# Performance work log

Measured on AMD Instinct MI355X. Metric: run time of the kernel, lower is better.

Reference implementation:

```python
import jax, jax.numpy as jnp
import numpy as np

RNN = 512
ENC = 512
HID = 512
ATT_SIZE = 196
B = 1024


def setup_inputs() -> dict:
    key = jax.random.key(0)
    ks = jax.random.split(key, 20)
    s = 0.02
    d = {
        "h": jax.random.normal(ks[0], (B, RNN), jnp.float32),
        "sentinel": jax.random.normal(ks[1], (B, RNN), jnp.float32),
        "att_feats": jax.random.normal(ks[2], (B, ATT_SIZE, RNN), jnp.float32),
        "W_ctx2att": jax.random.normal(ks[3], (RNN, HID), jnp.float32) * s,
        "b_ctx2att": jnp.zeros((HID,), jnp.float32),
        "W_sl": jax.random.normal(ks[4], (RNN, ENC), jnp.float32) * s,
        "b_sl": jnp.zeros((ENC,), jnp.float32),
        "W_se": jax.random.normal(ks[5], (ENC, HID), jnp.float32) * s,
        "b_se": jnp.zeros((HID,), jnp.float32),
        "W_hl": jax.random.normal(ks[6], (RNN, ENC), jnp.float32) * s,
        "b_hl": jnp.zeros((ENC,), jnp.float32),
        "W_he": jax.random.normal(ks[7], (ENC, HID), jnp.float32) * s,
        "b_he": jnp.zeros((HID,), jnp.float32),
        "W_alpha": jax.random.normal(ks[8], (HID, 1), jnp.float32) * s,
        "b_alpha": jnp.zeros((1,), jnp.float32),
        "W_att2h": jax.random.normal(ks[9], (RNN, RNN), jnp.float32) * s,
        "b_att2h": jnp.zeros((RNN,), jnp.float32),
    }
    return d


def reference(h, sentinel, att_feats, W_ctx2att, b_ctx2att, W_sl, b_sl,
              W_se, b_se, W_hl, b_hl, W_he, b_he, W_alpha, b_alpha,
              W_att2h, b_att2h):
    # Eval mode: dropout is identity.
    # Project attention features: [B, 196, HID]
    p_att = jnp.einsum("bsd,dh->bsh", att_feats, W_ctx2att) + b_ctx2att
    # Sentinel branch
    sent_lin = jax.nn.relu(sentinel @ W_sl + b_sl)          # [B, ENC]
    sent_emb = sent_lin @ W_se + b_se                       # [B, HID]
    # Hidden-state branch
    h_lin = jnp.tanh(h @ W_hl + b_hl)                       # [B, ENC]
    h_emb = h_lin @ W_he + b_he                             # [B, HID]
    # Concat sentinel with visual features: [B, 197, *]
    img_all = jnp.concatenate([sent_lin[:, None, :], att_feats], axis=1)
    img_all_embed = jnp.concatenate([sent_emb[:, None, :], p_att], axis=1)
    # Additive attention scores over 197 positions
    hA = jnp.tanh(img_all_embed + h_emb[:, None, :])        # [B, 197, HID]
    scores = (jnp.einsum("bsh,ho->bso", hA, W_alpha) + b_alpha)[..., 0]  # [B, 197]
    alpha = jax.nn.softmax(scores, axis=-1)
    # Weighted context
    cHat = jnp.einsum("bs,bsd->bd", alpha, img_all)          # [B, RNN]
    atten_out = cHat + h_lin
    out = jnp.tanh(atten_out @ W_att2h + b_att2h)            # [B, RNN]
    return out
```

## Files before the change

### kernel.cpp

```cpp
#include <hip/hip_runtime.h>
#include <hip/hip_bf16.h>

#define KDIM 512
#define NDIM 512
#define ATT  196
#define NB   1024

typedef __attribute__((ext_vector_type(8))) short bf16x8;
typedef __attribute__((ext_vector_type(8))) unsigned short ushort8;
typedef __attribute__((ext_vector_type(4))) float f32x4;

typedef const __attribute__((address_space(1))) unsigned int gas_uint;
typedef __attribute__((address_space(3))) unsigned int las_uint;

__device__ __forceinline__ void gload16(const void* g, void* l) {
    __builtin_amdgcn_global_load_lds((gas_uint*)g, (las_uint*)l, 16, 0, 0);
}

__device__ __forceinline__ float fast_tanh(float x) {
    x = fminf(15.f, fmaxf(-15.f, x));
    float t = __expf(2.f * x);
    return (t - 1.f) / (t + 1.f);
}

__device__ __forceinline__ unsigned short f2bf(float x) {
    union { float f; unsigned u; } v; v.f = x;
    unsigned r = v.u + 0x7FFF + ((v.u >> 16) & 1);
    return (unsigned short)(r >> 16);
}

__device__ __forceinline__ unsigned pk2(float a, float b) {
    __hip_bfloat162 h = __float22bfloat162_rn(float2{a, b});
    union { __hip_bfloat162 h2; unsigned u; } c; c.h2 = h;
    return c.u;
}

__global__ __launch_bounds__(256) void prep_weights(
        const float* __restrict__ W0, const float* __restrict__ W1,
        const float* __restrict__ W2, const float* __restrict__ W3,
        const float* __restrict__ W4, const float* __restrict__ W5,
        unsigned short* __restrict__ Wt) {
    int w = blockIdx.x >> 6;
    int t = blockIdx.x & 63;
    int k0 = (t >> 3) << 6, n0 = (t & 7) << 6;
    const float* W = (w == 0) ? W0 : (w == 1) ? W1 : (w == 2) ? W2 :
                     (w == 3) ? W3 : (w == 4) ? W4 : W5;
    __shared__ float tile[64][65];
    int tid = threadIdx.x;
    int nc = tid & 15, kr = tid >> 4;
#pragma unroll
    for (int i = 0; i < 4; ++i) {
        int k = kr + i * 16;
        float4 v = *(const float4*)&W[(size_t)(k0 + k) * NDIM + n0 + nc * 4];
        tile[k][nc * 4 + 0] = v.x; tile[k][nc * 4 + 1] = v.y;
        tile[k][nc * 4 + 2] = v.z; tile[k][nc * 4 + 3] = v.w;
    }
    __syncthreads();
    int n = tid >> 2, ks = tid & 3;
    ushort8 v0, v1;
#pragma unroll
    for (int j = 0; j < 8; ++j) v0[j] = f2bf(tile[ks * 16 + j][n]);
#pragma unroll
    for (int j = 0; j < 8; ++j) v1[j] = f2bf(tile[ks * 16 + 8 + j][n]);
    size_t base = ((size_t)w << 18) + (size_t)(n0 + n) * KDIM + k0 + ks * 16;
    *(ushort8*)&Wt[base] = v0;
    *(ushort8*)&Wt[base + 8] = v1;
}

__global__ __launch_bounds__(256) void gemm64(
        const float* __restrict__ A0, const unsigned short* __restrict__ W0,
        const float* __restrict__ bia0, float* __restrict__ O0, int act0,
        const float* __restrict__ A1, const unsigned short* __restrict__ W1,
        const float* __restrict__ bia1, float* __restrict__ O1, int act1) {
    const int op = blockIdx.y;
    const float* A = op ? A1 : A0;
    const unsigned short* Bt = op ? W1 : W0;
    const float* bias = op ? bia1 : bia0;
    float* out = op ? O1 : O0;
    const int act = op ? act1 : act0;

    __shared__ unsigned short A_lds[2][64 * 32];
    __shared__ unsigned short B_lds[2][128 * 32];

    const int tid = threadIdx.x;
    const int gm0 = (blockIdx.x >> 2) * 64, gn0 = (blockIdx.x & 3) * 128;
    const int wid = tid >> 6, lane = tid & 63;
    const int wm = wid >> 1, wn = wid & 1;
    const int lr = lane & 15, lk = lane >> 4;

    const int arow = tid >> 2, akc = tid & 3;
    const float* aptr = A + (size_t)(gm0 + arow) * KDIM + akc * 8;
    const int aoff = arow * 32 + ((akc ^ ((arow >> 1) & 3)) << 3);

    auto stageB = [&](int kt, int buf) {
#pragma unroll
        for (int j = 0; j < 2; ++j) {
            int c = tid + j * 256;
            int col = c >> 2, slot = c & 3;
            const unsigned short* src = Bt + (size_t)(gn0 + col) * KDIM +
                                        ((slot ^ ((col >> 1) & 3)) << 3) + kt * 32;
            gload16(src, &B_lds[buf][c * 8]);
        }
    };

    f32x4 acc[2][4] = {};

    {
        float4 x0 = *(const float4*)aptr;
        float4 x1 = *(const float4*)(aptr + 4);
        stageB(0, 0);
        uint4 p;
        p.x = pk2(x0.x, x0.y); p.y = pk2(x0.z, x0.w);
        p.z = pk2(x1.x, x1.y); p.w = pk2(x1.z, x1.w);
        *(uint4*)&A_lds[0][aoff] = p;
    }
    __syncthreads();

    const int swk = ((lk ^ ((lr >> 1) & 3)) << 3);
    for (int kt = 0; kt < 16; ++kt) {
        const int buf = kt & 1;
        float4 x0, x1;
        if (kt < 15) {
            const float* ap = aptr + (kt + 1) * 32;
            x0 = *(const float4*)ap;
            x1 = *(const float4*)(ap + 4);
            stageB(kt + 1, buf ^ 1);
        }
        bf16x8 af[2], bfr[4];
#pragma unroll
        for (int m = 0; m < 2; ++m)
            af[m] = *(const bf16x8*)&A_lds[buf][(wm * 32 + m * 16 + lr) * 32 + swk];
#pragma unroll
        for (int n = 0; n < 4; ++n)
            bfr[n] = *(const bf16x8*)&B_lds[buf][(wn * 64 + n * 16 + lr) * 32 + swk];
#pragma unroll
        for (int m = 0; m < 2; ++m)
#pragma unroll
            for (int n = 0; n < 4; ++n)
                acc[m][n] = __builtin_amdgcn_mfma_f32_16x16x32_bf16(af[m], bfr[n], acc[m][n], 0, 0, 0);
        if (kt < 15) {
            uint4 p;
            p.x = pk2(x0.x, x0.y); p.y = pk2(x0.z, x0.w);
            p.z = pk2(x1.x, x1.y); p.w = pk2(x1.z, x1.w);
            *(uint4*)&A_lds[buf ^ 1][aoff] = p;
        }
        __syncthreads();
    }

#pragma unroll
    for (int m = 0; m < 2; ++m)
#pragma unroll
        for (int n = 0; n < 4; ++n) {
            int col = gn0 + wn * 64 + n * 16 + lr;
            float bsv = bias[col];
#pragma unroll
            for (int r = 0; r < 4; ++r) {
                int row = gm0 + wm * 32 + m * 16 + lk * 4 + r;
                float v = acc[m][n][r] + bsv;
                if (act == 0) v = fmaxf(v, 0.f);
                else if (act == 1) v = fast_tanh(v);
                out[(size_t)row * NDIM + col] = v;
            }
        }
}

__launch_bounds__(256, 3)
__global__ void gemm_score(const float* __restrict__ A,
                           const unsigned short* __restrict__ Bt,
                           const float* __restrict__ b_ctx,
                           const float* __restrict__ h_emb,
                           const float* __restrict__ Walpha,
                           float* __restrict__ score) {
    __shared__ unsigned short A_lds[3][128 * 32];
    __shared__ unsigned short B_lds[3][128 * 32];
    __shared__ float ch_s[2][128];
    __shared__ float wa_s[128];
    __shared__ float s_red[2][128];

    const int tid  = threadIdx.x;
    const int bidx = blockIdx.x;
    const int xcd  = bidx & 7, u = bidx >> 3;
    const int mblk = xcd * 196 + (u >> 2), nblk = u & 3;
    const int gm0  = mblk * 128, gn0 = nblk * 128;

    const int wid = tid >> 6, lane = tid & 63;
    const int wm  = wid >> 1, wn = wid & 1;
    const int lr  = lane & 15, lk = lane >> 4;

    const int arow = tid >> 1, ahalf = tid & 1;
    const float* aptr = A + (size_t)(gm0 + arow) * KDIM + ahalf * 16;
    const int skc0  = (ahalf * 2) ^ ((arow >> 1) & 3);
    const int aoff0 = arow * 32 + skc0 * 8;
    const int aoff1 = arow * 32 + (skc0 ^ 1) * 8;

    const int c1 = tid + 256;
    const int bcol0 = tid >> 2, bk0 = (tid & 3) ^ ((bcol0 >> 1) & 3);
    const int bcol1 = c1 >> 2,  bk1 = (c1 & 3) ^ ((bcol1 >> 1) & 3);
    const unsigned short* bsrc0 = Bt + (size_t)(gn0 + bcol0) * KDIM + bk0 * 8;
    const unsigned short* bsrc1 = Bt + (size_t)(gn0 + bcol1) * KDIM + bk1 * 8;

    auto issueB = [&](int kt, int buf) {
        gload16(bsrc0 + kt * 32, &B_lds[buf][tid * 8]);
        gload16(bsrc1 + kt * 32, &B_lds[buf][c1 * 8]);
    };
    auto loadA = [&](int kt, float4* x) {
        const float* ap = aptr + kt * 32;
        x[0] = *(const float4*)(ap);
        x[1] = *(const float4*)(ap + 4);
        x[2] = *(const float4*)(ap + 8);
        x[3] = *(const float4*)(ap + 12);
    };
    auto writeA = [&](float4* x, int buf) {
        uint4 p0, p1;
        p0.x = pk2(x[0].x, x[0].y); p0.y = pk2(x[0].z, x[0].w);
        p0.z = pk2(x[1].x, x[1].y); p0.w = pk2(x[1].z, x[1].w);
        p1.x = pk2(x[2].x, x[2].y); p1.y = pk2(x[2].z, x[2].w);
        p1.z = pk2(x[3].x, x[3].y); p1.w = pk2(x[3].z, x[3].w);
        *(uint4*)&A_lds[buf][aoff0] = p0;
        *(uint4*)&A_lds[buf][aoff1] = p1;
    };

    f32x4 acc[4][4] = {};
    float4 xa[4], xb[4];
    const int swk = ((lk ^ ((lr >> 1) & 3)) << 3);

    loadA(0, xa);
    issueB(0, 0);
    writeA(xa, 0);
    loadA(1, xa);
    issueB(1, 1);
    asm volatile("s_waitcnt vmcnt(6) lgkmcnt(0)" ::: "memory");
    __builtin_amdgcn_sched_barrier(0);
    __builtin_amdgcn_s_barrier();
    __builtin_amdgcn_sched_barrier(0);

    auto body = [&](int t, int bT, int bT1, int bT2, float4* xc, float4* xn) {
        if (t + 2 < 16) {
            loadA(t + 2, xn);
            issueB(t + 2, bT2);
        }
        __builtin_amdgcn_sched_barrier(0);
        bf16x8 af[4], bfr[4];
#pragma unroll
        for (int m = 0; m < 4; ++m)
            af[m] = *(const bf16x8*)&A_lds[bT][(wm * 64 + m * 16 + lr) * 32 + swk];
#pragma unroll
        for (int n = 0; n < 4; ++n)
            bfr[n] = *(const bf16x8*)&B_lds[bT][(wn * 64 + n * 16 + lr) * 32 + swk];
#pragma unroll
        for (int m = 0; m < 4; ++m)
#pragma unroll
            for (int n = 0; n < 4; ++n)
                acc[m][n] = __builtin_amdgcn_mfma_f32_16x16x32_bf16(af[m], bfr[n], acc[m][n], 0, 0, 0);
        if (t + 1 < 16) writeA(xc, bT1);
        if (t < 15) {
            if (t + 2 < 16) {
                asm volatile("s_waitcnt vmcnt(6) lgkmcnt(0)" ::: "memory");
            } else {
                asm volatile("s_waitcnt vmcnt(0) lgkmcnt(0)" ::: "memory");
            }
            __builtin_amdgcn_sched_barrier(0);
            __builtin_amdgcn_s_barrier();
            __builtin_amdgcn_sched_barrier(0);
        }
    };

    int q0 = 0;
#pragma unroll 1
    for (int tt = 0; tt < 16; tt += 2) {
        int q1 = (q0 == 2) ? 0 : q0 + 1;
        int q2 = (q1 == 2) ? 0 : q1 + 1;
        int q3 = (q2 == 2) ? 0 : q2 + 1;
        body(tt,     q0, q1, q2, xa, xb);
        body(tt + 1, q1, q2, q3, xb, xa);
        q0 = q2;
    }

    const int bb0 = gm0 / ATT;
    {
        int j = tid >> 7, cloc = tid & 127;
        int bb = bb0 + j; if (bb > NB - 1) bb = NB - 1;
        ch_s[j][cloc] = b_ctx[gn0 + cloc] + h_emb[(size_t)bb * NDIM + gn0 + cloc];
        if (tid < 128) wa_s[tid] = Walpha[gn0 + tid];
    }
    __syncthreads();

    const int bsplit = (bb0 + 1) * ATT;
#pragma unroll
    for (int m = 0; m < 4; ++m) {
#pragma unroll
        for (int r = 0; r < 4; ++r) {
            int rloc = wm * 64 + m * 16 + lk * 4 + r;
            int rg = gm0 + rloc;
            int sel = (rg >= bsplit) ? 1 : 0;
            float sum = 0.f;
#pragma unroll
            for (int n = 0; n < 4; ++n) {
                int cloc = wn * 64 + n * 16 + lr;
                sum += fast_tanh(acc[m][n][r] + ch_s[sel][cloc]) * wa_s[cloc];
            }
            sum += __shfl_xor(sum, 1);
            sum += __shfl_xor(sum, 2);
            sum += __shfl_xor(sum, 4);
            sum += __shfl_xor(sum, 8);
            if (lr == 0) s_red[wn][rloc] = sum;
        }
    }
    __syncthreads();
    if (tid < 128) {
        float tot = s_red[0][tid] + s_red[1][tid];
        int rg = gm0 + tid;
        int sel = (rg >= bsplit) ? 1 : 0;
        int bb = bb0 + sel;
        atomicAdd(&score[(size_t)bb * 197 + (rg - bb * ATT) + 1], tot);
    }
}

__global__ __launch_bounds__(256) void softmax_chat(
        const float* __restrict__ score, const float* __restrict__ sent_emb,
        const float* __restrict__ h_emb, const float* __restrict__ Walpha,
        const float* __restrict__ sent_lin, const float* __restrict__ h_lin,
        const float* __restrict__ att, float* __restrict__ atten_out) {
    int b = blockIdx.x, tid = threadIdx.x;
    __shared__ float al[200];
    __shared__ float r4[4];

    float2 se = ((const float2*)(sent_emb + (size_t)b * NDIM))[tid];
    float2 he = ((const float2*)(h_emb + (size_t)b * NDIM))[tid];
    float2 wa = ((const float2*)Walpha)[tid];
    float val = fast_tanh(se.x + he.x) * wa.x + fast_tanh(se.y + he.y) * wa.y;
#pragma unroll
    for (int o = 32; o; o >>= 1) val += __shfl_xor(val, o);
    if ((tid & 63) == 0) r4[tid >> 6] = val;
    __syncthreads();
    float ssent = r4[0] + r4[1] + r4[2] + r4[3];
    __syncthreads();

    float v = -1e30f;
    if (tid < 197) v = (tid == 0) ? ssent : score[(size_t)b * 197 + tid];
    float m = v;
#pragma unroll
    for (int o = 32; o; o >>= 1) m = fmaxf(m, __shfl_xor(m, o));
    if ((tid & 63) == 0) r4[tid >> 6] = m;
    __syncthreads();
    m = fmaxf(fmaxf(r4[0], r4[1]), fmaxf(r4[2], r4[3]));
    __syncthreads();
    float e = (tid < 197) ? __expf(v - m) : 0.f;
    float s = e;
#pragma unroll
    for (int o = 32; o; o >>= 1) s += __shfl_xor(s, o);
    if ((tid & 63) == 0) r4[tid >> 6] = s;
    __syncthreads();
    s = r4[0] + r4[1] + r4[2] + r4[3];
    if (tid < 197) al[tid] = e / s;
    __syncthreads();

    const float2* af = (const float2*)(att + (size_t)b * ATT * KDIM);
    float2 a0 = ((const float2*)(sent_lin + (size_t)b * KDIM))[tid];
    float w0 = al[0];
    float2 accv; accv.x = w0 * a0.x; accv.y = w0 * a0.y;
#pragma unroll 14
    for (int ss = 0; ss < ATT; ++ss) {
        float w = al[ss + 1];
        float2 x = af[(size_t)ss * 256 + tid];
        accv.x += w * x.x; accv.y += w * x.y;
    }
    float2 hl = ((const float2*)(h_lin + (size_t)b * KDIM))[tid];
    accv.x += hl.x; accv.y += hl.y;
    ((float2*)(atten_out + (size_t)b * KDIM))[tid] = accv;
}

extern "C" void kernel_launch(void* const* d_in, const int* in_sizes, int n_in,
                              void* d_out, int out_size, void* d_ws, size_t ws_size,
                              hipStream_t stream) {
    const float* h     = (const float*)d_in[0];
    const float* sent  = (const float*)d_in[1];
    const float* att   = (const float*)d_in[2];
    const float* W_ctx = (const float*)d_in[3];
    const float* b_ctx = (const float*)d_in[4];
    const float* W_sl  = (const float*)d_in[5];
    const float* b_sl  = (const float*)d_in[6];
    const float* W_se  = (const float*)d_in[7];
    const float* b_se  = (const float*)d_in[8];
    const float* W_hl  = (const float*)d_in[9];
    const float* b_hl  = (const float*)d_in[10];
    const float* W_he  = (const float*)d_in[11];
    const float* b_he  = (const float*)d_in[12];
    const float* W_al  = (const float*)d_in[13];
    const float* W_a2h = (const float*)d_in[15];
    const float* b_a2h = (const float*)d_in[16];
    float* out = (float*)d_out;

    char* ws = (char*)d_ws;
    unsigned short* Wt = (unsigned short*)ws;
    float* sent_lin = (float*)(ws + 6u * 512 * 1024);
    float* h_lin    = sent_lin + (size_t)NB * 512;
    float* h_emb    = h_lin    + (size_t)NB * 512;
    float* sent_emb = h_emb    + (size_t)NB * 512;
    float* scorebuf = sent_emb + (size_t)NB * 512;
    float* atten    = scorebuf + (size_t)NB * 197;

    const size_t WSZ = 512 * 512;
    prep_weights<<<384, 256, 0, stream>>>(W_sl, W_hl, W_he, W_ctx, W_a2h, W_se, Wt);
    hipMemsetAsync(scorebuf, 0, (size_t)NB * 197 * sizeof(float), stream);

    gemm64<<<dim3(64, 2), 256, 0, stream>>>(
        sent, Wt + 0 * WSZ, b_sl, sent_lin, 0,
        h,    Wt + 1 * WSZ, b_hl, h_lin,    1);
    gemm64<<<dim3(64, 2), 256, 0, stream>>>(
        h_lin,    Wt + 2 * WSZ, b_he, h_emb,    2,
        sent_lin, Wt + 5 * WSZ, b_se, sent_emb, 2);

    gemm_score<<<6272, 256, 0, stream>>>(att, Wt + 3 * WSZ, b_ctx, h_emb, W_al, scorebuf);

    softmax_chat<<<NB, 256, 0, stream>>>(scorebuf, sent_emb, h_emb, W_al,
                                         sent_lin, h_lin, att, atten);

    gemm64<<<dim3(64, 1), 256, 0, stream>>>(
        atten, Wt + 4 * WSZ, b_a2h, out, 1,
        atten, Wt + 4 * WSZ, b_a2h, out, 1);
}
```

Measured before the change: 391.5 us.

## Keep full W_ctx2att column tile resident in LDS, loop blocks over four M-tiles

The score GEMM now loads the entire 512x128 bf16 weight slice for its N block into LDS once (128 KB) and reuses it across four consecutive 128-row M tiles. Each block runs a persistent-style loop with double-buffered A staging and an epilogue every 16 k-steps, and the grid shrinks by four times. This removes the repeated weight reloads and per-block prologue costs. In exchange occupancy drops to one block per CU and the weight load is exposed at block start without overlap.

```diff
diff --git a/kernel.cpp b/kernel.cpp
--- a/kernel.cpp
+++ b/kernel.cpp
@@ -164,155 +164,161 @@
         }
 }
 
-__launch_bounds__(256, 3)
+__launch_bounds__(256, 1)
 __global__ void gemm_score(const float* __restrict__ A,
                            const unsigned short* __restrict__ Bt,
                            const float* __restrict__ b_ctx,
                            const float* __restrict__ h_emb,
                            const float* __restrict__ Walpha,
                            float* __restrict__ score) {
-    __shared__ unsigned short A_lds[3][128 * 32];
-    __shared__ unsigned short B_lds[3][128 * 32];
-    __shared__ float ch_s[2][128];
-    __shared__ float wa_s[128];
+    __shared__ unsigned short B_res[16 * 4096];
+    __shared__ unsigned short A_buf[2][128 * 32];
     __shared__ float s_red[2][128];
 
-    const int tid  = threadIdx.x;
-    const int bidx = blockIdx.x;
-    const int xcd  = bidx & 7, u = bidx >> 3;
-    const int mblk = xcd * 196 + (u >> 2), nblk = u & 3;
-    const int gm0  = mblk * 128, gn0 = nblk * 128;
+    const int tid = threadIdx.x;
+    const int bid = blockIdx.x;
+    const int xcd = bid & 7, v = bid >> 3;
+    const int nblk = v & 3, gl = v >> 2;
+    const int group = xcd * 49 + gl;
+    const int gbase = group * 512;
+    const int gn0 = nblk * 128;
 
     const int wid = tid >> 6, lane = tid & 63;
-    const int wm  = wid >> 1, wn = wid & 1;
-    const int lr  = lane & 15, lk = lane >> 4;
+    const int wm = wid >> 1, wn = wid & 1;
+    const int lr = lane & 15, lk = lane >> 4;
+    const int swk = ((lk ^ ((lr >> 1) & 3)) << 3);
 
     const int arow = tid >> 1, ahalf = tid & 1;
-    const float* aptr = A + (size_t)(gm0 + arow) * KDIM + ahalf * 16;
-    const int skc0  = (ahalf * 2) ^ ((arow >> 1) & 3);
+    const int skc0 = (ahalf * 2) ^ ((arow >> 1) & 3);
     const int aoff0 = arow * 32 + skc0 * 8;
     const int aoff1 = arow * 32 + (skc0 ^ 1) * 8;
 
-    const int c1 = tid + 256;
-    const int bcol0 = tid >> 2, bk0 = (tid & 3) ^ ((bcol0 >> 1) & 3);
-    const int bcol1 = c1 >> 2,  bk1 = (c1 & 3) ^ ((bcol1 >> 1) & 3);
-    const unsigned short* bsrc0 = Bt + (size_t)(gn0 + bcol0) * KDIM + bk0 * 8;
-    const unsigned short* bsrc1 = Bt + (size_t)(gn0 + bcol1) * KDIM + bk1 * 8;
-
-    auto issueB = [&](int kt, int buf) {
-        gload16(bsrc0 + kt * 32, &B_lds[buf][tid * 8]);
-        gload16(bsrc1 + kt * 32, &B_lds[buf][c1 * 8]);
-    };
-    auto loadA = [&](int kt, float4* x) {
-        const float* ap = aptr + kt * 32;
-        x[0] = *(const float4*)(ap);
-        x[1] = *(const float4*)(ap + 4);
-        x[2] = *(const float4*)(ap + 8);
-        x[3] = *(const float4*)(ap + 12);
-    };
-    auto writeA = [&](float4* x, int buf) {
+    int cols[4];
+    float wav[4], bcv[4];
+#pragma unroll
+    for (int n = 0; n < 4; ++n) {
+        cols[n] = gn0 + wn * 64 + n * 16 + lr;
+        wav[n] = Walpha[cols[n]];
+        bcv[n] = b_ctx[cols[n]];
+    }
+    asm volatile("s_waitcnt vmcnt(0)" ::: "memory");
+    __builtin_amdgcn_sched_barrier(0);
+
+#pragma unroll
+    for (int i = 0; i < 32; ++i) {
+        int c = tid + i * 256;
+        int kt = c >> 9, w = c & 511;
+        int col = w >> 2, slot = w & 3;
+        int kc = slot ^ ((col >> 1) & 3);
+        gload16(Bt + (size_t)(gn0 + col) * KDIM + kt * 32 + kc * 8, &B_res[c * 8]);
+    }
+    __builtin_amdgcn_sched_barrier(0);
+
+    f32x4 acc[4][4] = {};
+    float4 xe0, xe1, xe2, xe3, xo0, xo1, xo2, xo3;
+
+    auto LOADA = [&](int s, float4& y0, float4& y1, float4& y2, float4& y3) {
+        const float* ap = A + (size_t)(gbase + ((s >> 4) << 7) + arow) * KDIM +
+                          ((s & 15) << 5) + ahalf * 16;
+        y0 = *(const float4*)(ap);
+        y1 = *(const float4*)(ap + 4);
+        y2 = *(const float4*)(ap + 8);
+        y3 = *(const float4*)(ap + 12);
+    };
+    auto CVTW = [&](const float4& y0, const float4& y1, const float4& y2,
+                    const float4& y3, int buf) {
         uint4 p0, p1;
-        p0.x = pk2(x[0].x, x[0].y); p0.y = pk2(x[0].z, x[0].w);
-        p0.z = pk2(x[1].x, x[1].y); p0.w = pk2(x[1].z, x[1].w);
-        p1.x = pk2(x[2].x, x[2].y); p1.y = pk2(x[2].z, x[2].w);
-        p1.z = pk2(x[3].x, x[3].y); p1.w = pk2(x[3].z, x[3].w);
-        *(uint4*)&A_lds[buf][aoff0] = p0;
-        *(uint4*)&A_lds[buf][aoff1] = p1;
-    };
-
-    f32x4 acc[4][4] = {};
-    float4 xa[4], xb[4];
-    const int swk = ((lk ^ ((lr >> 1) & 3)) << 3);
-
-    loadA(0, xa);
-    issueB(0, 0);
-    writeA(xa, 0);
-    loadA(1, xa);
-    issueB(1, 1);
-    asm volatile("s_waitcnt vmcnt(6) lgkmcnt(0)" ::: "memory");
-    __builtin_amdgcn_sched_barrier(0);
-    __builtin_amdgcn_s_barrier();
-    __builtin_amdgcn_sched_barrier(0);
-
-    auto body = [&](int t, int bT, int bT1, int bT2, float4* xc, float4* xn) {
-        if (t + 2 < 16) {
-            loadA(t + 2, xn);
-            issueB(t + 2, bT2);
-        }
-        __builtin_amdgcn_sched_barrier(0);
+        p0.x = pk2(y0.x, y0.y); p0.y = pk2(y0.z, y0.w);
+        p0.z = pk2(y1.x, y1.y); p0.w = pk2(y1.z, y1.w);
+        p1.x = pk2(y2.x, y2.y); p1.y = pk2(y2.z, y2.w);
+        p1.z = pk2(y3.x, y3.y); p1.w = pk2(y3.z, y3.w);
+        *(uint4*)&A_buf[buf][aoff0] = p0;
+        *(uint4*)&A_buf[buf][aoff1] = p1;
+    };
+    auto STEP = [&](int bufA, int kt) {
         bf16x8 af[4], bfr[4];
+        const unsigned short* bb = &B_res[kt * 4096];
+#pragma unroll
+        for (int n = 0; n < 4; ++n)
+            bfr[n] = *(const bf16x8*)&bb[(wn * 64 + n * 16 + lr) * 32 + swk];
 #pragma unroll
         for (int m = 0; m < 4; ++m)
-            af[m] = *(const bf16x8*)&A_lds[bT][(wm * 64 + m * 16 + lr) * 32 + swk];
-#pragma unroll
-        for (int n = 0; n < 4; ++n)
-            bfr[n] = *(const bf16x8*)&B_lds[bT][(wn * 64 + n * 16 + lr) * 32 + swk];
+            af[m] = *(const bf16x8*)&A_buf[bufA][(wm * 64 + m * 16 + lr) * 32 + swk];
 #pragma unroll
         for (int m = 0; m < 4; ++m)
 #pragma unroll
             for (int n = 0; n < 4; ++n)
                 acc[m][n] = __builtin_amdgcn_mfma_f32_16x16x32_bf16(af[m], bfr[n], acc[m][n], 0, 0, 0);
-        if (t + 1 < 16) writeA(xc, bT1);
-        if (t < 15) {
-            if (t + 2 < 16) {
-                asm volatile("s_waitcnt vmcnt(6) lgkmcnt(0)" ::: "memory");
-            } else {
-                asm volatile("s_waitcnt vmcnt(0) lgkmcnt(0)" ::: "memory");
+    };
+    auto BAR = [&]() {
+        asm volatile("s_waitcnt lgkmcnt(0)" ::: "memory");
+        __builtin_amdgcn_sched_barrier(0);
+        __builtin_amdgcn_s_barrier();
+        __builtin_amdgcn_sched_barrier(0);
+    };
+    auto EPILOGUE = [&](int mt) {
+        const int r0 = gbase + (mt << 7);
+        const int bb0 = r0 / ATT;
+        const int bsplit = (bb0 + 1) * ATT;
+        const int bb1 = (bb0 < NB - 1) ? bb0 + 1 : bb0;
+        float ch0[4], ch1[4];
+#pragma unroll
+        for (int n = 0; n < 4; ++n) {
+            ch0[n] = h_emb[(size_t)bb0 * NDIM + cols[n]] + bcv[n];
+            ch1[n] = h_emb[(size_t)bb1 * NDIM + cols[n]] + bcv[n];
+        }
+#pragma unroll
+        for (int m = 0; m < 4; ++m) {
+#pragma unroll
+            for (int r = 0; r < 4; ++r) {
+                const int rloc = wm * 64 + m * 16 + lk * 4 + r;
+                const int rg = r0 + rloc;
+                const bool hi = (rg >= bsplit);
+                float sum = 0.f;
+#pragma unroll
+                for (int n = 0; n < 4; ++n)
+                    sum += fast_tanh(acc[m][n][r] + (hi ? ch1[n] : ch0[n])) * wav[n];
+                sum += __shfl_xor(sum, 1);
+                sum += __shfl_xor(sum, 2);
+                sum += __shfl_xor(sum, 4);
+                sum += __shfl_xor(sum, 8);
+                if (lr == 0) s_red[wn][rloc] = sum;
             }
-            __builtin_amdgcn_sched_barrier(0);
-            __builtin_amdgcn_s_barrier();
-            __builtin_amdgcn_sched_barrier(0);
-        }
-    };
-
-    int q0 = 0;
+        }
+        BAR();
+        if (tid < 128) {
+            float tot = s_red[0][tid] + s_red[1][tid];
+            int rg = r0 + tid;
+            int bb = (rg >= bsplit) ? bb1 : bb0;
+            atomicAdd(&score[(size_t)bb * 197 + (rg - bb * ATT) + 1], tot);
+        }
+        BAR();
+#pragma unroll
+        for (int m = 0; m < 4; ++m)
+#pragma unroll
+            for (int n = 0; n < 4; ++n)
+                acc[m][n] = (f32x4){0.f, 0.f, 0.f, 0.f};
+    };
+
+    LOADA(0, xe0, xe1, xe2, xe3);
+    LOADA(1, xo0, xo1, xo2, xo3);
+    __builtin_amdgcn_sched_barrier(0);
+    CVTW(xe0, xe1, xe2, xe3, 0);
+    BAR();
+
 #pragma unroll 1
-    for (int tt = 0; tt < 16; tt += 2) {
-        int q1 = (q0 == 2) ? 0 : q0 + 1;
-        int q2 = (q1 == 2) ? 0 : q1 + 1;
-        int q3 = (q2 == 2) ? 0 : q2 + 1;
-        body(tt,     q0, q1, q2, xa, xb);
-        body(tt + 1, q1, q2, q3, xb, xa);
-        q0 = q2;
-    }
-
-    const int bb0 = gm0 / ATT;
-    {
-        int j = tid >> 7, cloc = tid & 127;
-        int bb = bb0 + j; if (bb > NB - 1) bb = NB - 1;
-        ch_s[j][cloc] = b_ctx[gn0 + cloc] + h_emb[(size_t)bb * NDIM + gn0 + cloc];
-        if (tid < 128) wa_s[tid] = Walpha[gn0 + tid];
-    }
-    __syncthreads();
-
-    const int bsplit = (bb0 + 1) * ATT;
-#pragma unroll
-    for (int m = 0; m < 4; ++m) {
-#pragma unroll
-        for (int r = 0; r < 4; ++r) {
-            int rloc = wm * 64 + m * 16 + lk * 4 + r;
-            int rg = gm0 + rloc;
-            int sel = (rg >= bsplit) ? 1 : 0;
-            float sum = 0.f;
-#pragma unroll
-            for (int n = 0; n < 4; ++n) {
-                int cloc = wn * 64 + n * 16 + lr;
-                sum += fast_tanh(acc[m][n][r] + ch_s[sel][cloc]) * wa_s[cloc];
-            }
-            sum += __shfl_xor(sum, 1);
-            sum += __shfl_xor(sum, 2);
-            sum += __shfl_xor(sum, 4);
-            sum += __shfl_xor(sum, 8);
-            if (lr == 0) s_red[wn][rloc] = sum;
-        }
-    }
-    __syncthreads();
-    if (tid < 128) {
-        float tot = s_red[0][tid] + s_red[1][tid];
-        int rg = gm0 + tid;
-        int sel = (rg >= bsplit) ? 1 : 0;
-        int bb = bb0 + sel;
-        atomicAdd(&score[(size_t)bb * 197 + (rg - bb * ATT) + 1], tot);
+    for (int i = 0; i < 32; ++i) {
+        if (i < 31) LOADA(2 * i + 2, xe0, xe1, xe2, xe3);
+        __builtin_amdgcn_sched_barrier(0);
+        STEP(0, (2 * i) & 15);
+        CVTW(xo0, xo1, xo2, xo3, 1);
+        BAR();
+        if (i < 31) LOADA(2 * i + 3, xo0, xo1, xo2, xo3);
+        __builtin_amdgcn_sched_barrier(0);
+        STEP(1, (2 * i + 1) & 15);
+        if (i < 31) CVTW(xe0, xe1, xe2, xe3, 0);
+        BAR();
+        if ((i & 7) == 7) EPILOGUE(i >> 3);
     }
 }
 
@@ -411,7 +417,7 @@
         h_lin,    Wt + 2 * WSZ, b_he, h_emb,    2,
         sent_lin, Wt + 5 * WSZ, b_se, sent_emb, 2);
 
-    gemm_score<<<6272, 256, 0, stream>>>(att, Wt + 3 * WSZ, b_ctx, h_emb, W_al, scorebuf);
+    gemm_score<<<1568, 256, 0, stream>>>(att, Wt + 3 * WSZ, b_ctx, h_emb, W_al, scorebuf);
 
     softmax_chat<<<NB, 256, 0, stream>>>(scorebuf, sent_emb, h_emb, W_al,
                                          sent_lin, h_lin, att, atten);
```

Result: slower. 693.4 us (+77.1%).
